# Performance work log

Hardware: AMD Instinct MI355X
Metric: run time of the kernel (lower is better)

## Reference

```python
import jax, jax.numpy as jnp
import numpy as np

KERNEL = 4  # conv kernel == stride (non-overlapping patches)


def _conv(x, W, b):
    # x: [B, Cin, H, W], W: [Cout, Cin, k, k] (OIHW), stride == kernel, VALID padding
    y = jax.lax.conv_general_dilated(
        x, W, window_strides=(KERNEL, KERNEL), padding='VALID',
        dimension_numbers=('NCHW', 'OIHW', 'NCHW'))
    return y + b[None, :, None, None]


def setup_inputs() -> dict:
    key = jax.random.key(0)
    ks = jax.random.split(key, 7)
    B, Cin, H, Wd = 4, 64, 256, 256
    Cout = 128
    s = 0.05
    return {
        'x': jax.random.normal(ks[0], (B, Cin, H, Wd), dtype=jnp.float32),
        'Wq': jax.random.normal(ks[1], (Cout, Cin, KERNEL, KERNEL), dtype=jnp.float32) * s,
        'bq': jax.random.normal(ks[2], (Cout,), dtype=jnp.float32) * s,
        'Wk': jax.random.normal(ks[3], (Cout, Cin, KERNEL, KERNEL), dtype=jnp.float32) * s,
        'bk': jax.random.normal(ks[4], (Cout,), dtype=jnp.float32) * s,
        'Wv': jax.random.normal(ks[5], (Cout, Cin, KERNEL, KERNEL), dtype=jnp.float32) * s,
        'bv': jax.random.normal(ks[6], (Cout,), dtype=jnp.float32) * s,
    }


def reference(x, Wq, bq, Wk, bk, Wv, bv):
    B = x.shape[0]
    q = _conv(x, Wq, bq)              # [B, O, Hp, Wp]
    O, Hp, Wp = q.shape[1], q.shape[2], q.shape[3]
    N = Hp * Wp
    q = q.reshape(B, O, N)
    k = _conv(x, Wk, bk).reshape(B, O, N)
    v = _conv(x, Wv, bv).reshape(B, O, N)
    # scores[b, n, m] = sum_o q[b,o,n] * k[b,o,m]  (NO scaling, as in original)
    scores = jnp.einsum('bon,bom->bnm', q, k)
    attn = jax.nn.softmax(scores, axis=-1)        # [B, N, N]
    # attended^T: out[b, o, n] = sum_m attn[b,n,m] * v[b,o,m]
    out = jnp.einsum('bnm,bom->bon', attn, v)
    return out.reshape(B, O, Hp, Wp)
```

## Files before the change

### kernel.cpp

```cpp
#include <hip/hip_runtime.h>
#include <cstdint>
#include <cstddef>

#define NB 4
#define NP 4096
#define OD 128

typedef _Float16 h16;
typedef _Float16 h16x8 __attribute__((ext_vector_type(8)));
typedef _Float16 h16x4 __attribute__((ext_vector_type(4)));
typedef float    f32x4 __attribute__((ext_vector_type(4)));

__device__ __forceinline__ void async16(const void* g, void* l) {
    __builtin_amdgcn_global_load_lds(
        (const __attribute__((address_space(1))) void*)g,
        (__attribute__((address_space(3))) void*)l, 16, 0, 0);
}

__global__ __launch_bounds__(256) void wcvt(
    const float* __restrict__ Wq, const float* __restrict__ Wk,
    const float* __restrict__ Wv, h16* __restrict__ W16s)
{
    int g = blockIdx.x * 256 + threadIdx.x;
    int mat = g >> 14, r = g & 16383;
    int kc = r >> 9, q = r & 511, o = q >> 2, csw = q & 3;
    int c = csw ^ ((o >> 1) & 3);
    const float* W = (mat == 0) ? Wq : (mat == 1) ? Wk : Wv;
    const float* src = W + (size_t)o * 1024 + kc * 32 + 8 * c;
    f32x4 a = *(const f32x4*)src;
    f32x4 b = *(const f32x4*)(src + 4);
    h16x8 h = {(h16)a.x, (h16)a.y, (h16)a.z, (h16)a.w,
               (h16)b.x, (h16)b.y, (h16)b.z, (h16)b.w};
    *(h16x8*)&W16s[(size_t)g * 8] = h;
}

__global__ __launch_bounds__(256, 2) void conv_qkv(
    const float* __restrict__ x, const h16* __restrict__ W16s,
    const float* __restrict__ bq, const float* __restrict__ bk,
    const float* __restrict__ bv,
    h16* __restrict__ qt, h16* __restrict__ kt, h16* __restrict__ vt)
{
    const int nt = blockIdx.x;
    const int b  = blockIdx.y;
    const int tid = threadIdx.x, lane = tid & 63, wv = tid >> 6;
    const int lr = lane & 15, qd = lane >> 4;
    const int o_w = 32 * wv;

    __shared__ __align__(16) char smem[85504];
    float* biasl = (float*)(smem + 83968);
    if (tid < 128) {
        biasl[tid] = bq[tid]; biasl[128 + tid] = bk[tid]; biasl[256 + tid] = bv[tid];
    }

    auto dmaW = [&](int kc, int bs) {
#pragma unroll
        for (int t = 0; t < 6; ++t) {
            int grp = wv * 6 + t;
            int mat = grp >> 3, sg = grp & 7;
            async16(W16s + ((size_t)(mat * 32 + kc) * 512 + sg * 64 + lane) * 8,
                    smem + bs * 24576 + mat * 8192 + sg * 1024);
        }
    };

    f32x4 xr[2][2];
    auto xload = [&](int kc, int sl) {
        int n = tid >> 2, kg = tid & 3;
        int c = kg >> 1, kh2 = (kg & 1) * 2;
        const float* p = &x[(((size_t)(b * 64 + 2 * kc + c) * 256) + 4 * nt + kh2) * 256 + 4 * n];
        xr[sl][0] = *(const f32x4*)p;
        xr[sl][1] = *(const f32x4*)(p + 256);
    };
    auto xwrite = [&](int sl, int xbs) {
        int n = tid >> 2, kg = tid & 3;
        int c = kg >> 1, kh2 = (kg & 1) * 2;
        h16x8 h = {(h16)xr[sl][0].x, (h16)xr[sl][0].y, (h16)xr[sl][0].z, (h16)xr[sl][0].w,
                   (h16)xr[sl][1].x, (h16)xr[sl][1].y, (h16)xr[sl][1].z, (h16)xr[sl][1].w};
        *(h16x8*)(smem + 73728 + xbs * 5120 + n * 80 + c * 32 + kh2 * 8) = h;
    };

    f32x4 acc[3][2][4];
#pragma unroll
    for (int m = 0; m < 3; ++m)
#pragma unroll
        for (int a = 0; a < 2; ++a)
#pragma unroll
            for (int c = 0; c < 4; ++c) acc[m][a][c] = (f32x4){0.f, 0.f, 0.f, 0.f};

    xload(0, 0); dmaW(0, 0);
    xload(1, 1); dmaW(1, 1);
    xwrite(0, 0);
    __syncthreads();

    int wb = 0;
#pragma unroll 2
    for (int kc = 0; kc < 32; ++kc) {
        int xbs = kc & 1;
        if (kc + 2 < 32) {
            dmaW(kc + 2, (wb == 0) ? 2 : wb - 1);
            xload(kc + 2, xbs);
        }
        const h16* Xl = (const h16*)(smem + 73728 + xbs * 5120);
        const char* Wl = smem + wb * 24576;

        h16x8 bf[4];
#pragma unroll
        for (int tn = 0; tn < 4; ++tn)
            bf[tn] = *(const h16x8*)&Xl[(16 * tn + lr) * 40 + 8 * qd];
#pragma unroll
        for (int mat = 0; mat < 3; ++mat) {
            h16x8 af[2];
#pragma unroll
            for (int to = 0; to < 2; ++to) {
                int o = o_w + 16 * to + lr;
                af[to] = *(const h16x8*)(Wl + mat * 8192 + (size_t)(o * 4 + (qd ^ ((o >> 1) & 3))) * 16);
            }
#pragma unroll
            for (int to = 0; to < 2; ++to)
#pragma unroll
                for (int tn = 0; tn < 4; ++tn)
                    acc[mat][to][tn] = __builtin_amdgcn_mfma_f32_16x16x32_f16(af[to], bf[tn], acc[mat][to][tn], 0, 0, 0);
        }
        if (kc + 1 < 32) xwrite((kc + 1) & 1, 1 - xbs);
        wb = (wb == 2) ? 0 : wb + 1;
        __syncthreads();
    }

    const int n0 = nt * 64;
#pragma unroll
    for (int mat = 0; mat < 2; ++mat) {
        h16* bnc = (h16*)smem;
#pragma unroll
        for (int to = 0; to < 2; ++to)
#pragma unroll
            for (int tn = 0; tn < 4; ++tn) {
                int ob = o_w + 16 * to + 4 * qd;
                int n  = 16 * tn + lr;
                h16x4 hv = {(h16)(acc[mat][to][tn][0] + biasl[mat * 128 + ob]),
                            (h16)(acc[mat][to][tn][1] + biasl[mat * 128 + ob + 1]),
                            (h16)(acc[mat][to][tn][2] + biasl[mat * 128 + ob + 2]),
                            (h16)(acc[mat][to][tn][3] + biasl[mat * 128 + ob + 3])};
                *(h16x4*)&bnc[n * 136 + ob] = hv;
            }
        __syncthreads();
        h16* dst = mat ? kt : qt;
#pragma unroll
        for (int j = 0; j < 4; ++j) {
            int s = tid + 256 * j;
            int n = s >> 4, oc = s & 15;
            *(h16x8*)(dst + ((size_t)(b * NP + n0 + n)) * OD + 8 * oc) = *(h16x8*)&bnc[n * 136 + 8 * oc];
        }
        __syncthreads();
    }
    {
        h16* bnc = (h16*)smem;
#pragma unroll
        for (int to = 0; to < 2; ++to)
#pragma unroll
            for (int tn = 0; tn < 4; ++tn)
#pragma unroll
                for (int r = 0; r < 4; ++r) {
                    int o = o_w + 16 * to + 4 * qd + r;
                    int n = 16 * tn + lr;
                    bnc[o * 72 + n] = (h16)(acc[2][to][tn][r] + biasl[256 + o]);
                }
        __syncthreads();
#pragma unroll
        for (int j = 0; j < 4; ++j) {
            int s = tid + 256 * j;
            int o = s >> 3, ch = s & 7;
            int g = ch >> 2, q2 = ch & 3;
            h16x8 hv;
#pragma unroll
            for (int r2 = 0; r2 < 8; ++r2) {
                int mt = r2 >> 2, r = r2 & 3;
                hv[r2] = bnc[o * 72 + 32 * g + 16 * mt + 4 * q2 + r];
            }
            *(h16x8*)(vt + ((size_t)(b * OD + o)) * NP + n0 + 32 * g + 8 * q2) = hv;
        }
    }
}

template <int SP>
__global__ __launch_bounds__(256, 3) void flash_attn(
    const h16* __restrict__ qt, const h16* __restrict__ kt,
    const h16* __restrict__ vt, h16* __restrict__ po, float2* __restrict__ ml)
{
    constexpr int MR  = NP / SP;
    constexpr int NIT = MR / 32;
    const int nt = blockIdx.x, sp = blockIdx.y, b = blockIdx.z;
    const int tid = threadIdx.x, lane = tid & 63, wv = tid >> 6;
    const int lr = lane & 15, qd = lane >> 4;

    __shared__ __align__(16) char smem[32768];

    h16x8 qf[2][4];
#pragma unroll
    for (int rt = 0; rt < 2; ++rt)
#pragma unroll
        for (int kc = 0; kc < 4; ++kc)
            qf[rt][kc] = *(const h16x8*)&qt[((size_t)(b * NP + nt * 128 + 32 * wv + 16 * rt + lr)) * OD
                                            + 32 * kc + 8 * qd];

    float m_run[2] = {-1e30f, -1e30f}, l_run[2] = {0.f, 0.f};
    f32x4 oacc[2][8];
#pragma unroll
    for (int rt = 0; rt < 2; ++rt)
#pragma unroll
        for (int t = 0; t < 8; ++t) oacc[rt][t] = (f32x4){0.f, 0.f, 0.f, 0.f};

    auto dma = [&](int it, int bs) {
        int m0 = sp * MR + it * 32;
#pragma unroll
        for (int t = 0; t < 2; ++t) {
            int s = wv * 128 + t * 64 + lane;
            int m = s >> 4, cst = s & 15, csrc = cst ^ (m & 15);
            async16(kt + ((size_t)(b * NP + m0 + m)) * OD + 8 * csrc,
                    smem + bs * 8192 + (wv * 128 + t * 64) * 16);
        }
#pragma unroll
        for (int t = 0; t < 2; ++t) {
            int s = wv * 128 + t * 64 + lane;
            int o = s >> 2, cst = s & 3, csrc = cst ^ ((o >> 1) & 3);
            async16(vt + ((size_t)(b * OD + o)) * NP + m0 + 8 * csrc,
                    smem + 16384 + bs * 8192 + (wv * 128 + t * 64) * 16);
        }
    };

    dma(0, 0);
    __syncthreads();

#pragma unroll 2
    for (int it = 0; it < NIT; ++it) {
        int c = it & 1;
        if (it + 1 < NIT) dma(it + 1, 1 - c);
        const h16* Kb = (const h16*)(smem + c * 8192);
        const h16* Vb = (const h16*)(smem + 16384 + c * 8192);

        f32x4 sc[2][2];
#pragma unroll
        for (int rt = 0; rt < 2; ++rt)
#pragma unroll
            for (int mt = 0; mt < 2; ++mt) sc[rt][mt] = (f32x4){0.f, 0.f, 0.f, 0.f};
#pragma unroll
        for (int mt = 0; mt < 2; ++mt)
#pragma unroll
            for (int kc = 0; kc < 4; ++kc) {
                h16x8 kf = *(const h16x8*)&Kb[(size_t)((16 * mt + lr) * 16 + ((4 * kc + qd) ^ lr)) * 8];
                sc[0][mt] = __builtin_amdgcn_mfma_f32_16x16x32_f16(kf, qf[0][kc], sc[0][mt], 0, 0, 0);
                sc[1][mt] = __builtin_amdgcn_mfma_f32_16x16x32_f16(kf, qf[1][kc], sc[1][mt], 0, 0, 0);
            }

        h16x4 pf[2][2];
        float al[2];
#pragma unroll
        for (int rt = 0; rt < 2; ++rt) {
            float mx = fmaxf(fmaxf(fmaxf(sc[rt][0][0], sc[rt][0][1]), fmaxf(sc[rt][0][2], sc[rt][0][3])),
                             fmaxf(fmaxf(sc[rt][1][0], sc[rt][1][1]), fmaxf(sc[rt][1][2], sc[rt][1][3])));
            mx = fmaxf(mx, __shfl_xor(mx, 16));
            mx = fmaxf(mx, __shfl_xor(mx, 32));
            float mn = fmaxf(m_run[rt], mx);
            al[rt] = __expf(m_run[rt] - mn);
            m_run[rt] = mn;
            float rs = 0.f;
#pragma unroll
            for (int mt = 0; mt < 2; ++mt)
#pragma unroll
                for (int r = 0; r < 4; ++r) {
                    float e = __expf(sc[rt][mt][r] - mn);
                    sc[rt][mt][r] = e;
                    rs += e;
                }
            rs += __shfl_xor(rs, 16);
            rs += __shfl_xor(rs, 32);
            l_run[rt] = l_run[rt] * al[rt] + rs;
            pf[rt][0] = (h16x4){(h16)sc[rt][0][0], (h16)sc[rt][0][1], (h16)sc[rt][0][2], (h16)sc[rt][0][3]};
            pf[rt][1] = (h16x4){(h16)sc[rt][1][0], (h16)sc[rt][1][1], (h16)sc[rt][1][2], (h16)sc[rt][1][3]};
        }
#pragma unroll
        for (int rt = 0; rt < 2; ++rt)
#pragma unroll
            for (int to = 0; to < 8; ++to)
#pragma unroll
                for (int r = 0; r < 4; ++r) oacc[rt][to][r] *= al[rt];

#pragma unroll
        for (int to = 0; to < 8; ++to) {
            int o = 16 * to + lr;
            h16x8 vv = *(const h16x8*)&Vb[(size_t)(o * 4 + (qd ^ ((o >> 1) & 3))) * 8];
            h16x4 va = __builtin_shufflevector(vv, vv, 0, 1, 2, 3);
            h16x4 vb2 = __builtin_shufflevector(vv, vv, 4, 5, 6, 7);
#pragma unroll
            for (int rt = 0; rt < 2; ++rt) {
                oacc[rt][to] = __builtin_amdgcn_mfma_f32_16x16x16f16(va,  pf[rt][0], oacc[rt][to], 0, 0, 0);
                oacc[rt][to] = __builtin_amdgcn_mfma_f32_16x16x16f16(vb2, pf[rt][1], oacc[rt][to], 0, 0, 0);
            }
        }
        __syncthreads();
    }

    const size_t nbase = (size_t)(sp * NB + b) * NP + nt * 128 + 32 * wv;
    if (qd == 0) {
#pragma unroll
        for (int rt = 0; rt < 2; ++rt)
            ml[nbase + 16 * rt + lr] = make_float2(m_run[rt], l_run[rt]);
    }
    float inv[2] = {1.f / l_run[0], 1.f / l_run[1]};
#pragma unroll
    for (int rt = 0; rt < 2; ++rt)
#pragma unroll
        for (int to = 0; to < 8; ++to) {
            h16x4 hv = {(h16)(oacc[rt][to][0] * inv[rt]), (h16)(oacc[rt][to][1] * inv[rt]),
                        (h16)(oacc[rt][to][2] * inv[rt]), (h16)(oacc[rt][to][3] * inv[rt])};
            *(h16x4*)&po[(nbase + 16 * rt + lr) * OD + 16 * to + 4 * qd] = hv;
        }
}

template <int SP>
__global__ __launch_bounds__(256) void combine(
    const h16* __restrict__ po, const float2* __restrict__ ml,
    float* __restrict__ out)
{
    const int nt = blockIdx.x, b = blockIdx.y;
    const int n0 = nt * 64, tid = threadIdx.x;
    __shared__ float w[SP][64];
    __shared__ float bn[64 * 130];

    if (tid < 64) {
        int n = n0 + tid;
        float m[SP], l[SP], M = -1e30f;
#pragma unroll
        for (int s = 0; s < SP; ++s) {
            float2 v = ml[(size_t)(s * NB + b) * NP + n];
            m[s] = v.x; l[s] = v.y;
            M = fmaxf(M, m[s]);
        }
        float d = 0.f, e[SP];
#pragma unroll
        for (int s = 0; s < SP; ++s) { e[s] = l[s] * __expf(m[s] - M); d += e[s]; }
        float id = 1.f / d;
#pragma unroll
        for (int s = 0; s < SP; ++s) w[s][tid] = e[s] * id;
    }
    __syncthreads();

#pragma unroll
    for (int j = 0; j < 4; ++j) {
        int s = tid + 256 * j;
        int n = s >> 4, oc = s & 15;
        float acc[8];
#pragma unroll
        for (int k = 0; k < 8; ++k) acc[k] = 0.f;
#pragma unroll
        for (int sp = 0; sp < SP; ++sp) {
            h16x8 v = *(const h16x8*)&po[((size_t)(sp * NB + b) * NP + n0 + n) * OD + 8 * oc];
            float ww = w[sp][n];
#pragma unroll
            for (int k = 0; k < 8; ++k) acc[k] += ww * (float)v[k];
        }
#pragma unroll
        for (int k = 0; k < 8; ++k) bn[n * 130 + 8 * oc + k] = acc[k];
    }
    __syncthreads();

#pragma unroll
    for (int j = 0; j < 8; ++j) {
        int s = tid + 256 * j;
        int o = s >> 4, n4 = s & 15;
        f32x4 r = {bn[(4 * n4 + 0) * 130 + o], bn[(4 * n4 + 1) * 130 + o],
                   bn[(4 * n4 + 2) * 130 + o], bn[(4 * n4 + 3) * 130 + o]};
        *(f32x4*)&out[((size_t)(b * OD + o)) * NP + n0 + 4 * n4] = r;
    }
}

extern "C" void kernel_launch(void* const* d_in, const int* in_sizes, int n_in,
                              void* d_out, int out_size, void* d_ws, size_t ws_size,
                              hipStream_t stream) {
    const float* x  = (const float*)d_in[0];
    const float* Wq = (const float*)d_in[1];
    const float* bq = (const float*)d_in[2];
    const float* Wk = (const float*)d_in[3];
    const float* bk = (const float*)d_in[4];
    const float* Wv = (const float*)d_in[5];
    const float* bv = (const float*)d_in[6];

    h16* qtp  = (h16*)d_ws;
    h16* ktp  = qtp + (size_t)NB * NP * OD;
    h16* vtp  = ktp + (size_t)NB * NP * OD;
    h16* W16s = vtp + (size_t)NB * NP * OD;
    h16* po   = W16s + (size_t)3 * 32 * 512 * 8;
    float* out = (float*)d_out;

    wcvt<<<dim3(192), 256, 0, stream>>>(Wq, Wk, Wv, W16s);
    conv_qkv<<<dim3(64, NB), 256, 0, stream>>>(x, W16s, bq, bk, bv, qtp, ktp, vtp);

    const size_t base = 13369344;
    const size_t need8 = base + (size_t)8 * NB * NP * OD * 2 + (size_t)8 * NB * NP * 8;
    if (ws_size >= need8) {
        float2* ml = (float2*)(po + (size_t)8 * NB * NP * OD);
        flash_attn<8><<<dim3(32, 8, NB), 256, 0, stream>>>(qtp, ktp, vtp, po, ml);
        combine<8><<<dim3(64, NB), 256, 0, stream>>>(po, ml, out);
    } else {
        float2* ml = (float2*)(po + (size_t)4 * NB * NP * OD);
        flash_attn<4><<<dim3(32, 4, NB), 256, 0, stream>>>(qtp, ktp, vtp, po, ml);
        combine<4><<<dim3(64, NB), 256, 0, stream>>>(po, ml, out);
    }
}
```

Baseline: 205.0 us.

## Fold log2e into Q, use exp2, widen PV MFMA, retune conv and combine

Q is pre-scaled by log2(e) in the conv epilogue so the softmax can use the native exp2 instruction instead of __expf. The PV product now uses 16x16x32 MFMAs on a K row permutation and a new V swizzle, so the V fragment no longer has to be split into halves. The conv weight buffer drops from triple to double buffering, which shrinks LDS and simplifies the V transpose store. The combine kernel uses smaller tiles with more blocks, flash_attn's launch-bounds occupancy goes from 3 to 4, and packed RTZ conversions replace the default rounding, which slightly lowers precision.

```diff
diff --git a/kernel.cpp b/kernel.cpp
--- a/kernel.cpp
+++ b/kernel.cpp
@@ -5,16 +5,26 @@
 #define NB 4
 #define NP 4096
 #define OD 128
+#define LOG2E 1.44269504f
 
 typedef _Float16 h16;
 typedef _Float16 h16x8 __attribute__((ext_vector_type(8)));
 typedef _Float16 h16x4 __attribute__((ext_vector_type(4)));
+typedef _Float16 h16x2 __attribute__((ext_vector_type(2)));
 typedef float    f32x4 __attribute__((ext_vector_type(4)));
 
 __device__ __forceinline__ void async16(const void* g, void* l) {
     __builtin_amdgcn_global_load_lds(
         (const __attribute__((address_space(1))) void*)g,
         (__attribute__((address_space(3))) void*)l, 16, 0, 0);
+}
+
+__device__ __forceinline__ h16x8 pack8(f32x4 a, f32x4 b) {
+    h16x2 p0 = __builtin_bit_cast(h16x2, __builtin_amdgcn_cvt_pkrtz(a[0], a[1]));
+    h16x2 p1 = __builtin_bit_cast(h16x2, __builtin_amdgcn_cvt_pkrtz(a[2], a[3]));
+    h16x2 p2 = __builtin_bit_cast(h16x2, __builtin_amdgcn_cvt_pkrtz(b[0], b[1]));
+    h16x2 p3 = __builtin_bit_cast(h16x2, __builtin_amdgcn_cvt_pkrtz(b[2], b[3]));
+    return (h16x8){p0[0], p0[1], p1[0], p1[1], p2[0], p2[1], p3[0], p3[1]};
 }
 
 __global__ __launch_bounds__(256) void wcvt(
@@ -46,8 +56,8 @@
     const int lr = lane & 15, qd = lane >> 4;
     const int o_w = 32 * wv;
 
-    __shared__ __align__(16) char smem[85504];
-    float* biasl = (float*)(smem + 83968);
+    __shared__ __align__(16) char smem[60928];
+    float* biasl = (float*)(smem + 59392);
     if (tid < 128) {
         biasl[tid] = bq[tid]; biasl[128 + tid] = bk[tid]; biasl[256 + tid] = bv[tid];
     }
@@ -75,7 +85,7 @@
         int c = kg >> 1, kh2 = (kg & 1) * 2;
         h16x8 h = {(h16)xr[sl][0].x, (h16)xr[sl][0].y, (h16)xr[sl][0].z, (h16)xr[sl][0].w,
                    (h16)xr[sl][1].x, (h16)xr[sl][1].y, (h16)xr[sl][1].z, (h16)xr[sl][1].w};
-        *(h16x8*)(smem + 73728 + xbs * 5120 + n * 80 + c * 32 + kh2 * 8) = h;
+        *(h16x8*)(smem + 49152 + xbs * 5120 + n * 80 + c * 32 + kh2 * 8) = h;
     };
 
     f32x4 acc[3][2][4];
@@ -87,20 +97,17 @@
             for (int c = 0; c < 4; ++c) acc[m][a][c] = (f32x4){0.f, 0.f, 0.f, 0.f};
 
     xload(0, 0); dmaW(0, 0);
-    xload(1, 1); dmaW(1, 1);
+    xload(1, 1);
     xwrite(0, 0);
     __syncthreads();
 
-    int wb = 0;
-#pragma unroll 2
     for (int kc = 0; kc < 32; ++kc) {
-        int xbs = kc & 1;
-        if (kc + 2 < 32) {
-            dmaW(kc + 2, (wb == 0) ? 2 : wb - 1);
-            xload(kc + 2, xbs);
-        }
-        const h16* Xl = (const h16*)(smem + 73728 + xbs * 5120);
-        const char* Wl = smem + wb * 24576;
+        int c = kc & 1;
+        if (kc + 1 < 32) dmaW(kc + 1, 1 - c);
+        if (kc + 2 < 32) xload(kc + 2, c);
+
+        const h16* Xl = (const h16*)(smem + 49152 + c * 5120);
+        const char* Wl = smem + c * 24576;
 
         h16x8 bf[4];
 #pragma unroll
@@ -120,8 +127,7 @@
                 for (int tn = 0; tn < 4; ++tn)
                     acc[mat][to][tn] = __builtin_amdgcn_mfma_f32_16x16x32_f16(af[to], bf[tn], acc[mat][to][tn], 0, 0, 0);
         }
-        if (kc + 1 < 32) xwrite((kc + 1) & 1, 1 - xbs);
-        wb = (wb == 2) ? 0 : wb + 1;
+        if (kc + 1 < 32) xwrite((kc + 1) & 1, 1 - c);
         __syncthreads();
     }
 
@@ -129,16 +135,17 @@
 #pragma unroll
     for (int mat = 0; mat < 2; ++mat) {
         h16* bnc = (h16*)smem;
+        const float qs = (mat == 0) ? LOG2E : 1.0f;
 #pragma unroll
         for (int to = 0; to < 2; ++to)
 #pragma unroll
             for (int tn = 0; tn < 4; ++tn) {
                 int ob = o_w + 16 * to + 4 * qd;
                 int n  = 16 * tn + lr;
-                h16x4 hv = {(h16)(acc[mat][to][tn][0] + biasl[mat * 128 + ob]),
-                            (h16)(acc[mat][to][tn][1] + biasl[mat * 128 + ob + 1]),
-                            (h16)(acc[mat][to][tn][2] + biasl[mat * 128 + ob + 2]),
-                            (h16)(acc[mat][to][tn][3] + biasl[mat * 128 + ob + 3])};
+                h16x4 hv = {(h16)((acc[mat][to][tn][0] + biasl[mat * 128 + ob]) * qs),
+                            (h16)((acc[mat][to][tn][1] + biasl[mat * 128 + ob + 1]) * qs),
+                            (h16)((acc[mat][to][tn][2] + biasl[mat * 128 + ob + 2]) * qs),
+                            (h16)((acc[mat][to][tn][3] + biasl[mat * 128 + ob + 3]) * qs)};
                 *(h16x4*)&bnc[n * 136 + ob] = hv;
             }
         __syncthreads();
@@ -168,20 +175,13 @@
         for (int j = 0; j < 4; ++j) {
             int s = tid + 256 * j;
             int o = s >> 3, ch = s & 7;
-            int g = ch >> 2, q2 = ch & 3;
-            h16x8 hv;
-#pragma unroll
-            for (int r2 = 0; r2 < 8; ++r2) {
-                int mt = r2 >> 2, r = r2 & 3;
-                hv[r2] = bnc[o * 72 + 32 * g + 16 * mt + 4 * q2 + r];
-            }
-            *(h16x8*)(vt + ((size_t)(b * OD + o)) * NP + n0 + 32 * g + 8 * q2) = hv;
+            *(h16x8*)(vt + ((size_t)(b * OD + o)) * NP + n0 + 8 * ch) = *(h16x8*)&bnc[o * 72 + 8 * ch];
         }
     }
 }
 
 template <int SP>
-__global__ __launch_bounds__(256, 3) void flash_attn(
+__global__ __launch_bounds__(256, 4) void flash_attn(
     const h16* __restrict__ qt, const h16* __restrict__ kt,
     const h16* __restrict__ vt, h16* __restrict__ po, float2* __restrict__ ml)
 {
@@ -213,14 +213,15 @@
 #pragma unroll
         for (int t = 0; t < 2; ++t) {
             int s = wv * 128 + t * 64 + lane;
-            int m = s >> 4, cst = s & 15, csrc = cst ^ (m & 15);
-            async16(kt + ((size_t)(b * NP + m0 + m)) * OD + 8 * csrc,
+            int l = s >> 4, cst = s & 15, csrc = cst ^ (l & 15);
+            int m = m0 + 8 * ((l >> 2) & 3) + 4 * (l >> 4) + (l & 3);
+            async16(kt + ((size_t)(b * NP + m)) * OD + 8 * csrc,
                     smem + bs * 8192 + (wv * 128 + t * 64) * 16);
         }
 #pragma unroll
         for (int t = 0; t < 2; ++t) {
             int s = wv * 128 + t * 64 + lane;
-            int o = s >> 2, cst = s & 3, csrc = cst ^ ((o >> 1) & 3);
+            int o = s >> 2, cst = s & 3, csrc = cst ^ ((o & 3) ^ ((o >> 2) & 3));
             async16(vt + ((size_t)(b * OD + o)) * NP + m0 + 8 * csrc,
                     smem + 16384 + bs * 8192 + (wv * 128 + t * 64) * 16);
         }
@@ -229,7 +230,6 @@
     dma(0, 0);
     __syncthreads();
 
-#pragma unroll 2
     for (int it = 0; it < NIT; ++it) {
         int c = it & 1;
         if (it + 1 < NIT) dma(it + 1, 1 - c);
@@ -250,7 +250,7 @@
                 sc[1][mt] = __builtin_amdgcn_mfma_f32_16x16x32_f16(kf, qf[1][kc], sc[1][mt], 0, 0, 0);
             }
 
-        h16x4 pf[2][2];
+        h16x8 pf[2];
         float al[2];
 #pragma unroll
         for (int rt = 0; rt < 2; ++rt) {
@@ -259,22 +259,21 @@
             mx = fmaxf(mx, __shfl_xor(mx, 16));
             mx = fmaxf(mx, __shfl_xor(mx, 32));
             float mn = fmaxf(m_run[rt], mx);
-            al[rt] = __expf(m_run[rt] - mn);
+            al[rt] = __builtin_amdgcn_exp2f(m_run[rt] - mn);
             m_run[rt] = mn;
             float rs = 0.f;
 #pragma unroll
             for (int mt = 0; mt < 2; ++mt)
 #pragma unroll
                 for (int r = 0; r < 4; ++r) {
-                    float e = __expf(sc[rt][mt][r] - mn);
+                    float e = __builtin_amdgcn_exp2f(sc[rt][mt][r] - mn);
                     sc[rt][mt][r] = e;
                     rs += e;
                 }
             rs += __shfl_xor(rs, 16);
             rs += __shfl_xor(rs, 32);
             l_run[rt] = l_run[rt] * al[rt] + rs;
-            pf[rt][0] = (h16x4){(h16)sc[rt][0][0], (h16)sc[rt][0][1], (h16)sc[rt][0][2], (h16)sc[rt][0][3]};
-            pf[rt][1] = (h16x4){(h16)sc[rt][1][0], (h16)sc[rt][1][1], (h16)sc[rt][1][2], (h16)sc[rt][1][3]};
+            pf[rt] = pack8(sc[rt][0], sc[rt][1]);
         }
 #pragma unroll
         for (int rt = 0; rt < 2; ++rt)
@@ -286,14 +285,9 @@
 #pragma unroll
         for (int to = 0; to < 8; ++to) {
             int o = 16 * to + lr;
-            h16x8 vv = *(const h16x8*)&Vb[(size_t)(o * 4 + (qd ^ ((o >> 1) & 3))) * 8];
-            h16x4 va = __builtin_shufflevector(vv, vv, 0, 1, 2, 3);
-            h16x4 vb2 = __builtin_shufflevector(vv, vv, 4, 5, 6, 7);
-#pragma unroll
-            for (int rt = 0; rt < 2; ++rt) {
-                oacc[rt][to] = __builtin_amdgcn_mfma_f32_16x16x16f16(va,  pf[rt][0], oacc[rt][to], 0, 0, 0);
-                oacc[rt][to] = __builtin_amdgcn_mfma_f32_16x16x16f16(vb2, pf[rt][1], oacc[rt][to], 0, 0, 0);
-            }
+            h16x8 va = *(const h16x8*)&Vb[(size_t)(o * 4 + (qd ^ ((o & 3) ^ ((o >> 2) & 3)))) * 8];
+            oacc[0][to] = __builtin_amdgcn_mfma_f32_16x16x32_f16(va, pf[0], oacc[0][to], 0, 0, 0);
+            oacc[1][to] = __builtin_amdgcn_mfma_f32_16x16x32_f16(va, pf[1], oacc[1][to], 0, 0, 0);
         }
         __syncthreads();
     }
@@ -321,11 +315,11 @@
     float* __restrict__ out)
 {
     const int nt = blockIdx.x, b = blockIdx.y;
-    const int n0 = nt * 64, tid = threadIdx.x;
-    __shared__ float w[SP][64];
-    __shared__ float bn[64 * 130];
-
-    if (tid < 64) {
+    const int n0 = nt * 32, tid = threadIdx.x;
+    __shared__ float w[SP][32];
+    __shared__ float bn[32 * 137];
+
+    if (tid < 32) {
         int n = n0 + tid;
         float m[SP], l[SP], M = -1e30f;
 #pragma unroll
@@ -336,7 +330,7 @@
         }
         float d = 0.f, e[SP];
 #pragma unroll
-        for (int s = 0; s < SP; ++s) { e[s] = l[s] * __expf(m[s] - M); d += e[s]; }
+        for (int s = 0; s < SP; ++s) { e[s] = l[s] * __builtin_amdgcn_exp2f(m[s] - M); d += e[s]; }
         float id = 1.f / d;
 #pragma unroll
         for (int s = 0; s < SP; ++s) w[s][tid] = e[s] * id;
@@ -344,7 +338,7 @@
     __syncthreads();
 
 #pragma unroll
-    for (int j = 0; j < 4; ++j) {
+    for (int j = 0; j < 2; ++j) {
         int s = tid + 256 * j;
         int n = s >> 4, oc = s & 15;
         float acc[8];
@@ -358,17 +352,17 @@
             for (int k = 0; k < 8; ++k) acc[k] += ww * (float)v[k];
         }
 #pragma unroll
-        for (int k = 0; k < 8; ++k) bn[n * 130 + 8 * oc + k] = acc[k];
+        for (int k = 0; k < 8; ++k) bn[n * 137 + 8 * oc + k] = acc[k];
     }
     __syncthreads();
 
 #pragma unroll
-    for (int j = 0; j < 8; ++j) {
+    for (int j = 0; j < 4; ++j) {
         int s = tid + 256 * j;
-        int o = s >> 4, n4 = s & 15;
-        f32x4 r = {bn[(4 * n4 + 0) * 130 + o], bn[(4 * n4 + 1) * 130 + o],
-                   bn[(4 * n4 + 2) * 130 + o], bn[(4 * n4 + 3) * 130 + o]};
-        *(f32x4*)&out[((size_t)(b * OD + o)) * NP + n0 + 4 * n4] = r;
+        int o = s >> 3, ng = s & 7;
+        f32x4 r = {bn[(4 * ng + 0) * 137 + o], bn[(4 * ng + 1) * 137 + o],
+                   bn[(4 * ng + 2) * 137 + o], bn[(4 * ng + 3) * 137 + o]};
+        *(f32x4*)&out[((size_t)(b * OD + o)) * NP + n0 + 4 * ng] = r;
     }
 }
 
@@ -398,10 +392,10 @@
     if (ws_size >= need8) {
         float2* ml = (float2*)(po + (size_t)8 * NB * NP * OD);
         flash_attn<8><<<dim3(32, 8, NB), 256, 0, stream>>>(qtp, ktp, vtp, po, ml);
-        combine<8><<<dim3(64, NB), 256, 0, stream>>>(po, ml, out);
+        combine<8><<<dim3(128, NB), 256, 0, stream>>>(po, ml, out);
     } else {
         float2* ml = (float2*)(po + (size_t)4 * NB * NP * OD);
         flash_attn<4><<<dim3(32, 4, NB), 256, 0, stream>>>(qtp, ktp, vtp, po, ml);
-        combine<4><<<dim3(64, NB), 256, 0, stream>>>(po, ml, out);
-    }
-}
+        combine<4><<<dim3(128, NB), 256, 0, stream>>>(po, ml, out);
+    }
+}
```

Result: slower. 272.6 us (+32.9%).
